# Optimization experiments

Measured on AMD Instinct MI355X. Metric: run time of the kernel, lower is better.

## Reference

```python
import jax, jax.numpy as jnp
import numpy as np

N = 100000
E = 1600000
NFEAT, NHID, NCLASS = 500, 128, 40


def setup_inputs() -> dict:
    key = jax.random.key(0)
    ks = jax.random.split(key, 12)
    x = jax.random.normal(ks[0], (N, NFEAT), dtype=jnp.float32)
    row = jax.random.randint(ks[1], (E,), 0, N, dtype=jnp.int32)
    col = jax.random.randint(ks[2], (E,), 0, N, dtype=jnp.int32)
    # precomputed normalized adjacency values (D^-1/2 A D^-1/2 style)
    edge_weight = jax.random.uniform(ks[3], (E,), dtype=jnp.float32) / 16.0
    def lin(k, fi, fo):
        s = 1.0 / np.sqrt(fi)
        return jax.random.uniform(k, (fi, fo), dtype=jnp.float32, minval=-s, maxval=s)
    return {
        "x": x, "row": row, "col": col, "edge_weight": edge_weight,
        "W1": lin(ks[4], NFEAT, NHID), "b1": jnp.zeros((NHID,), jnp.float32),
        "W2": lin(ks[5], NHID, NHID), "b2": jnp.zeros((NHID,), jnp.float32),
        "W3": lin(ks[6], NHID, NHID), "b3": jnp.zeros((NHID,), jnp.float32),
        "W4": lin(ks[7], NHID, NCLASS), "b4": jnp.zeros((NCLASS,), jnp.float32),
    }


def gcn_layer(h, row, col, edge_weight, W, b):
    # support = h @ W ; out = spmm(adj, support) + b  (Kipf GraphConvolution)
    support = h @ W                                   # [N, Fout]
    msgs = edge_weight[:, None] * support[col]        # [E, Fout] gather on source nodes
    agg = jax.ops.segment_sum(msgs, row, num_segments=N)  # scatter-add to dest nodes
    return agg + b


def reference(x, row, col, edge_weight, W1, b1, W2, b2, W3, b3, W4, b4):
    # dropout is identity in eval mode (training=False)
    h = jax.nn.relu(gcn_layer(x, row, col, edge_weight, W1, b1))
    h = jax.nn.relu(gcn_layer(h, row, col, edge_weight, W2, b2))
    h = jax.nn.relu(gcn_layer(h, row, col, edge_weight, W3, b3))
    h = gcn_layer(h, row, col, edge_weight, W4, b4)
    return jax.nn.log_softmax(h, axis=1)
```

## Files before the change

kernel.cpp:

```cpp
#include <hip/hip_runtime.h>
#include <cstdint>
#include <cstddef>

#define NFEAT 500
#define NHID  128
#define NCLASS 40

typedef __attribute__((ext_vector_type(8))) short bf16x8;
typedef __attribute__((ext_vector_type(4))) float f32x4;

__device__ __forceinline__ unsigned short f2bf(float f) {
    union { float f; unsigned u; } v; v.f = f;
    unsigned u = v.u;
    unsigned r = u + 0x7FFF + ((u >> 16) & 1);
    return (unsigned short)(r >> 16);
}
__device__ __forceinline__ float bf2f(unsigned short h) {
    union { unsigned u; float f; } v; v.u = ((unsigned)h) << 16; return v.f;
}


__global__ void k_hist(const int* __restrict__ row, int E, int* __restrict__ counts) {
    int i = blockIdx.x * 256 + threadIdx.x;
    if (i < E) atomicAdd(&counts[row[i]], 1);
}

__global__ void k_block_sum(const int* __restrict__ counts, int n, int* __restrict__ partials) {
    __shared__ int tmp[256];
    int i = blockIdx.x * 256 + threadIdx.x;
    tmp[threadIdx.x] = (i < n) ? counts[i] : 0;
    __syncthreads();
    for (int o = 128; o > 0; o >>= 1) {
        if (threadIdx.x < o) tmp[threadIdx.x] += tmp[threadIdx.x + o];
        __syncthreads();
    }
    if (threadIdx.x == 0) partials[blockIdx.x] = tmp[0];
}

__global__ void k_scan_partials(int* __restrict__ partials, int nb) {
    __shared__ int tmp[512];
    int t = threadIdx.x;
    int v = (t < nb) ? partials[t] : 0;
    tmp[t] = v;
    __syncthreads();
    for (int o = 1; o < 512; o <<= 1) {
        int add = (t >= o) ? tmp[t - o] : 0;
        __syncthreads();
        tmp[t] += add;
        __syncthreads();
    }
    if (t < nb) partials[t] = tmp[t] - v;
}

__global__ void k_scan_counts(int* __restrict__ counts, const int* __restrict__ partials,
                              int* __restrict__ row_ptr, int n) {
    __shared__ int tmp[256];
    int t = threadIdx.x;
    int i = blockIdx.x * 256 + t;
    int v = (i < n) ? counts[i] : 0;
    tmp[t] = v;
    __syncthreads();
    for (int o = 1; o < 256; o <<= 1) {
        int add = (t >= o) ? tmp[t - o] : 0;
        __syncthreads();
        tmp[t] += add;
        __syncthreads();
    }
    int incl = tmp[t];
    int base = partials[blockIdx.x];
    if (i < n) {
        row_ptr[i] = base + incl - v;
        counts[i] = 0;
    }
    if (i == n - 1) row_ptr[n] = base + incl;
}

__global__ void k_scatter(const int* __restrict__ row, const int* __restrict__ col,
                          const float* __restrict__ w, int E,
                          const int* __restrict__ row_ptr, int* __restrict__ cursor,
                          uint2* __restrict__ csr_cw) {
    int i = blockIdx.x * 256 + threadIdx.x;
    if (i < E) {
        int r = row[i];
        int p = row_ptr[r] + atomicAdd(&cursor[r], 1);
        csr_cw[p] = make_uint2((unsigned)col[i], __float_as_uint(w[i]));
    }
}


__global__ void k_prep_w(const float* __restrict__ W, unsigned short* __restrict__ Wt,
                         int K, int Norig, int Nt, int Kpad) {
    int idx = blockIdx.x * 256 + threadIdx.x;
    if (idx >= Nt * Kpad) return;
    int n = idx / Kpad, k = idx % Kpad;
    unsigned short v = 0;
    if (k < K && n < Norig) v = f2bf(W[(size_t)k * Norig + n]);
    Wt[idx] = v;
}


template<bool AFP32, int BN, int CN, int CPITCH>
__global__ __launch_bounds__(256) void k_gemm_mfma(const void* __restrict__ Ain,
                                                   const unsigned short* __restrict__ Wt,
                                                   unsigned short* __restrict__ C,
                                                   int M, int K, int Kpad) {
    constexpr int P  = 40;
    constexpr int NW = (BN == 128) ? 2 : 1;
    constexpr int MW = 4 / NW;
    constexpr int TM = 128 / (MW * 16);
    constexpr int TN = BN / (NW * 16);
    __shared__ unsigned short As[2][128][P];

    const int t = threadIdx.x;
    const int lane = t & 63;
    const int w = t >> 6;
    const int wm = w / NW, wn = w % NW;
    const int mbase = blockIdx.x * 128;
    const int l15 = lane & 15, quad = lane >> 4;

    const float* Af = (const float*)Ain;
    const unsigned short* Ab = (const unsigned short*)Ain;

    f32x4 acc[TM][TN];
#pragma unroll
    for (int mi = 0; mi < TM; mi++)
#pragma unroll
        for (int ni = 0; ni < TN; ni++)
            acc[mi][ni] = (f32x4){0.f, 0.f, 0.f, 0.f};

    float4 ra_f[4];
    uint4  ra_b[2];

    auto loadA = [&](int k0) {
        if (AFP32) {
#pragma unroll
            for (int p = 0; p < 4; p++) {
                int idx = p * 256 + t;
                int m = idx >> 3, ch = idx & 7;
                int gm = mbase + m, gk = k0 + ch * 4;
                float4 v = make_float4(0.f, 0.f, 0.f, 0.f);
                if (gm < M && gk + 4 <= K) v = *(const float4*)(Af + (size_t)gm * K + gk);
                ra_f[p] = v;
            }
        } else {
#pragma unroll
            for (int p = 0; p < 2; p++) {
                int idx = p * 256 + t;
                int m = idx >> 2, ch = idx & 3;
                ra_b[p] = *(const uint4*)(Ab + (size_t)(mbase + m) * Kpad + k0 + ch * 8);
            }
        }
    };
    auto storeLDS = [&](int buf) {
        if (AFP32) {
#pragma unroll
            for (int p = 0; p < 4; p++) {
                int idx = p * 256 + t;
                int m = idx >> 3, ch = idx & 7;
                float4 v = ra_f[p];
                unsigned long long pk = (unsigned long long)f2bf(v.x)
                                      | ((unsigned long long)f2bf(v.y) << 16)
                                      | ((unsigned long long)f2bf(v.z) << 32)
                                      | ((unsigned long long)f2bf(v.w) << 48);
                *(unsigned long long*)&As[buf][m][ch * 4] = pk;
            }
        } else {
#pragma unroll
            for (int p = 0; p < 2; p++) {
                int idx = p * 256 + t;
                int m = idx >> 2, ch = idx & 3;
                *(uint4*)&As[buf][m][ch * 8] = ra_b[p];
            }
        }
    };

    const int nIter = Kpad >> 5;
    loadA(0);
    storeLDS(0);
    __syncthreads();

    for (int it = 0; it < nIter; it++) {
        const int cur = it & 1;
        const int k0 = it << 5;
        const bool more = (it + 1) < nIter;
        if (more) loadA(k0 + 32);

        bf16x8 bfr[TN];
#pragma unroll
        for (int ni = 0; ni < TN; ni++)
            bfr[ni] = *(const bf16x8*)(Wt + (size_t)(wn * (TN * 16) + ni * 16 + l15) * Kpad + k0 + quad * 8);

        bf16x8 afr[TM];
#pragma unroll
        for (int mi = 0; mi < TM; mi++)
            afr[mi] = *(const bf16x8*)&As[cur][wm * (TM * 16) + mi * 16 + l15][quad * 8];

#pragma unroll
        for (int mi = 0; mi < TM; mi++)
#pragma unroll
            for (int ni = 0; ni < TN; ni++)
                acc[mi][ni] = __builtin_amdgcn_mfma_f32_16x16x32_bf16(afr[mi], bfr[ni], acc[mi][ni], 0, 0, 0);

        if (more) {
            storeLDS(cur ^ 1);
            __syncthreads();
        }
    }

#pragma unroll
    for (int mi = 0; mi < TM; mi++) {
#pragma unroll
        for (int r = 0; r < 4; r++) {
            int gm = mbase + wm * (TM * 16) + mi * 16 + quad * 4 + r;
#pragma unroll
            for (int ni = 0; ni < TN; ni++) {
                int gn = wn * (TN * 16) + ni * 16 + l15;
                if (gn < CN) C[(size_t)gm * CPITCH + gn] = f2bf(acc[mi][ni][r]);
            }
        }
    }
}


__global__ __launch_bounds__(256) void k_spmm128(const unsigned short* __restrict__ S,
                                                 const int* __restrict__ rp,
                                                 const uint2* __restrict__ cw,
                                                 const float* __restrict__ bias,
                                                 unsigned short* __restrict__ out,
                                                 int n, int do_relu) {
    int wid  = threadIdx.x >> 6;
    int lane = threadIdx.x & 63;
    int node = blockIdx.x * 4 + wid;
    if (node >= n) return;
    int s = rp[node], e = rp[node + 1];
    float a0x = 0.f, a0y = 0.f, a1x = 0.f, a1y = 0.f;
    float a2x = 0.f, a2y = 0.f, a3x = 0.f, a3y = 0.f;
    int i = s;
    for (; i + 4 <= e; i += 4) {
        uint2 e0 = cw[i], e1 = cw[i + 1], e2 = cw[i + 2], e3 = cw[i + 3];
        unsigned v0 = ((const unsigned*)(S + (size_t)e0.x * NHID))[lane];
        unsigned v1 = ((const unsigned*)(S + (size_t)e1.x * NHID))[lane];
        unsigned v2 = ((const unsigned*)(S + (size_t)e2.x * NHID))[lane];
        unsigned v3 = ((const unsigned*)(S + (size_t)e3.x * NHID))[lane];
        float w0 = __uint_as_float(e0.y), w1 = __uint_as_float(e1.y);
        float w2 = __uint_as_float(e2.y), w3 = __uint_as_float(e3.y);
        a0x = fmaf(w0, bf2f((unsigned short)v0), a0x); a0y = fmaf(w0, bf2f((unsigned short)(v0 >> 16)), a0y);
        a1x = fmaf(w1, bf2f((unsigned short)v1), a1x); a1y = fmaf(w1, bf2f((unsigned short)(v1 >> 16)), a1y);
        a2x = fmaf(w2, bf2f((unsigned short)v2), a2x); a2y = fmaf(w2, bf2f((unsigned short)(v2 >> 16)), a2y);
        a3x = fmaf(w3, bf2f((unsigned short)v3), a3x); a3y = fmaf(w3, bf2f((unsigned short)(v3 >> 16)), a3y);
    }
    for (; i < e; i++) {
        uint2 e0 = cw[i];
        unsigned v0 = ((const unsigned*)(S + (size_t)e0.x * NHID))[lane];
        float w0 = __uint_as_float(e0.y);
        a0x = fmaf(w0, bf2f((unsigned short)v0), a0x); a0y = fmaf(w0, bf2f((unsigned short)(v0 >> 16)), a0y);
    }
    float ax = (a0x + a1x) + (a2x + a3x) + bias[lane * 2];
    float ay = (a0y + a1y) + (a2y + a3y) + bias[lane * 2 + 1];
    if (do_relu) {
        ax = fmaxf(ax, 0.f);
        ay = fmaxf(ay, 0.f);
    }
    unsigned o = (unsigned)f2bf(ax) | ((unsigned)f2bf(ay) << 16);
    __builtin_nontemporal_store(o, (unsigned*)(out + (size_t)node * NHID) + lane);
}


__global__ __launch_bounds__(256) void k_spmm40_lsm(const unsigned short* __restrict__ S,
                                                    const int* __restrict__ rp,
                                                    const uint2* __restrict__ cw,
                                                    const float* __restrict__ bias,
                                                    float* __restrict__ out,
                                                    int n) {
    int wid  = threadIdx.x >> 6;
    int lane = threadIdx.x & 63;
    int node = blockIdx.x * 4 + wid;
    if (node >= n) return;
    int s = rp[node], e = rp[node + 1];
    float a0 = 0.f, a1 = 0.f, a2 = 0.f, a3 = 0.f;
    int i = s;
    bool act = lane < NCLASS;
    for (; i + 4 <= e; i += 4) {
        uint2 e0 = cw[i], e1 = cw[i + 1], e2 = cw[i + 2], e3 = cw[i + 3];
        if (act) {
            float v0 = bf2f(S[(size_t)e0.x * NCLASS + lane]);
            float v1 = bf2f(S[(size_t)e1.x * NCLASS + lane]);
            float v2 = bf2f(S[(size_t)e2.x * NCLASS + lane]);
            float v3 = bf2f(S[(size_t)e3.x * NCLASS + lane]);
            a0 = fmaf(__uint_as_float(e0.y), v0, a0);
            a1 = fmaf(__uint_as_float(e1.y), v1, a1);
            a2 = fmaf(__uint_as_float(e2.y), v2, a2);
            a3 = fmaf(__uint_as_float(e3.y), v3, a3);
        }
    }
    for (; i < e; i++) {
        uint2 e0 = cw[i];
        if (act) a0 = fmaf(__uint_as_float(e0.y), bf2f(S[(size_t)e0.x * NCLASS + lane]), a0);
    }
    float acc = (a0 + a1) + (a2 + a3);
    float logit = act ? acc + bias[lane] : -INFINITY;
    float m = logit;
#pragma unroll
    for (int o = 32; o >= 1; o >>= 1) m = fmaxf(m, __shfl_xor(m, o, 64));
    float ex = act ? expf(logit - m) : 0.f;
    float ssum = ex;
#pragma unroll
    for (int o = 32; o >= 1; o >>= 1) ssum += __shfl_xor(ssum, o, 64);
    if (act) {
        float r = logit - m - logf(ssum);
        __builtin_nontemporal_store(r, out + (size_t)node * NCLASS + lane);
    }
}


extern "C" void kernel_launch(void* const* d_in, const int* in_sizes, int n_in,
                              void* d_out, int out_size, void* d_ws, size_t ws_size,
                              hipStream_t stream) {
    const float* x  = (const float*)d_in[0];
    const int* row  = (const int*)d_in[1];
    const int* col  = (const int*)d_in[2];
    const float* ew = (const float*)d_in[3];
    const float* W1 = (const float*)d_in[4];
    const float* b1 = (const float*)d_in[5];
    const float* W2 = (const float*)d_in[6];
    const float* b2 = (const float*)d_in[7];
    const float* W3 = (const float*)d_in[8];
    const float* b3 = (const float*)d_in[9];
    const float* W4 = (const float*)d_in[10];
    const float* b4 = (const float*)d_in[11];
    float* out = (float*)d_out;

    const int Nn = in_sizes[0] / NFEAT;
    const int E  = in_sizes[1];
    const int NB = (Nn + 255) / 256;
    const int Mpad = (Nn + 127) & ~127;

    char* ws = (char*)d_ws;
    size_t off = 0;
    auto alloc = [&](size_t bytes) {
        size_t o = off;
        off = (off + bytes + 255) & ~(size_t)255;
        return o;
    };
    int*   row_ptr  = (int*)(ws + alloc((size_t)(Nn + 1) * 4));
    int*   counts   = (int*)(ws + alloc((size_t)Nn * 4));
    int*   partials = (int*)(ws + alloc((size_t)NB * 4));
    uint2* csr_cw   = (uint2*)(ws + alloc((size_t)E * 8));
    unsigned short* Sb  = (unsigned short*)(ws + alloc((size_t)Mpad * NHID * 2));
    unsigned short* Hb  = (unsigned short*)(ws + alloc((size_t)Mpad * NHID * 2));
    unsigned short* S4b = (unsigned short*)(ws + alloc((size_t)Mpad * NCLASS * 2));
    unsigned short* Wt1 = (unsigned short*)(ws + alloc((size_t)128 * 512 * 2));
    unsigned short* Wt2 = (unsigned short*)(ws + alloc((size_t)128 * 128 * 2));
    unsigned short* Wt3 = (unsigned short*)(ws + alloc((size_t)128 * 128 * 2));
    unsigned short* Wt4 = (unsigned short*)(ws + alloc((size_t)48 * 128 * 2));

    k_prep_w<<<(128 * 512 + 255) / 256, 256, 0, stream>>>(W1, Wt1, NFEAT, NHID, 128, 512);
    k_prep_w<<<(128 * 128 + 255) / 256, 256, 0, stream>>>(W2, Wt2, NHID, NHID, 128, 128);
    k_prep_w<<<(128 * 128 + 255) / 256, 256, 0, stream>>>(W3, Wt3, NHID, NHID, 128, 128);
    k_prep_w<<<(48 * 128 + 255) / 256, 256, 0, stream>>>(W4, Wt4, NHID, NCLASS, 48, 128);

    (void)hipMemsetAsync(counts, 0, (size_t)Nn * 4, stream);
    k_hist<<<(E + 255) / 256, 256, 0, stream>>>(row, E, counts);
    k_block_sum<<<NB, 256, 0, stream>>>(counts, Nn, partials);
    k_scan_partials<<<1, 512, 0, stream>>>(partials, NB);
    k_scan_counts<<<NB, 256, 0, stream>>>(counts, partials, row_ptr, Nn);
    k_scatter<<<(E + 255) / 256, 256, 0, stream>>>(row, col, ew, E, row_ptr, counts, csr_cw);

    const int gblocks = Mpad / 128;
    const int spmm_blocks = (Nn + 3) / 4;

    k_gemm_mfma<true, 128, 128, 128><<<gblocks, 256, 0, stream>>>(x, Wt1, Sb, Nn, NFEAT, 512);
    k_spmm128<<<spmm_blocks, 256, 0, stream>>>(Sb, row_ptr, csr_cw, b1, Hb, Nn, 1);
    k_gemm_mfma<false, 128, 128, 128><<<gblocks, 256, 0, stream>>>(Hb, Wt2, Sb, Nn, NHID, NHID);
    k_spmm128<<<spmm_blocks, 256, 0, stream>>>(Sb, row_ptr, csr_cw, b2, Hb, Nn, 1);
    k_gemm_mfma<false, 128, 128, 128><<<gblocks, 256, 0, stream>>>(Hb, Wt3, Sb, Nn, NHID, NHID);
    k_spmm128<<<spmm_blocks, 256, 0, stream>>>(Sb, row_ptr, csr_cw, b3, Hb, Nn, 1);
    k_gemm_mfma<false, 48, 40, 40><<<gblocks, 256, 0, stream>>>(Hb, Wt4, S4b, Nn, NHID, NHID);
    k_spmm40_lsm<<<spmm_blocks, 256, 0, stream>>>(S4b, row_ptr, csr_cw, b4, out, Nn);
}
```

Baseline: 860.1 us.

## Replace LDS-staged GEMM with direct register-fragment loads and double buffering

The GEMM no longer stages A tiles through shared memory with barriers. Each wave now loads its own MFMA A and B fragments straight from global memory into registers, with a two-set register double buffer, and computes a 32xBN slice covering the full N width. K is made a template constant so the loop can be fully unrolled. This removes LDS traffic and __syncthreads but makes each wave read all of W itself, and it relies on the cache for the strided per-lane row loads.

Result: slower. 893.2 us (+3.8%).

```diff
diff --git a/kernel.cpp b/kernel.cpp
--- a/kernel.cpp
+++ b/kernel.cpp
@@ -99,24 +99,19 @@
 }
 
 
-template<bool AFP32, int BN, int CN, int CPITCH>
-__global__ __launch_bounds__(256) void k_gemm_mfma(const void* __restrict__ Ain,
-                                                   const unsigned short* __restrict__ Wt,
-                                                   unsigned short* __restrict__ C,
-                                                   int M, int K, int Kpad) {
-    constexpr int P  = 40;
-    constexpr int NW = (BN == 128) ? 2 : 1;
-    constexpr int MW = 4 / NW;
-    constexpr int TM = 128 / (MW * 16);
-    constexpr int TN = BN / (NW * 16);
-    __shared__ unsigned short As[2][128][P];
-
+template<bool AFP32, int KPAD, int BN, int CN, int CPITCH>
+__global__ __launch_bounds__(256) void k_gemm_direct(const void* __restrict__ Ain,
+                                                     const unsigned short* __restrict__ Wt,
+                                                     unsigned short* __restrict__ C,
+                                                     int M, int K) {
+    constexpr int TM = 2;
+    constexpr int TN = BN / 16;
+    constexpr int NIT = KPAD / 32;
     const int t = threadIdx.x;
     const int lane = t & 63;
     const int w = t >> 6;
-    const int wm = w / NW, wn = w % NW;
-    const int mbase = blockIdx.x * 128;
     const int l15 = lane & 15, quad = lane >> 4;
+    const int rbase = blockIdx.x * 128 + w * 32;
 
     const float* Af = (const float*)Ain;
     const unsigned short* Ab = (const unsigned short*)Ain;
@@ -128,93 +123,77 @@
         for (int ni = 0; ni < TN; ni++)
             acc[mi][ni] = (f32x4){0.f, 0.f, 0.f, 0.f};
 
-    float4 ra_f[4];
-    uint4  ra_b[2];
-
-    auto loadA = [&](int k0) {
+    int rowi[TM];
+#pragma unroll
+    for (int mi = 0; mi < TM; mi++) {
+        int r = rbase + mi * 16 + l15;
+        rowi[mi] = AFP32 ? min(r, M - 1) : r;
+    }
+
+    float4 fA[2][TM][2];
+    bf16x8 hA[2][TM];
+    bf16x8 hB[2][TN];
+
+    auto loadA = [&](int set, int k0) {
         if (AFP32) {
-#pragma unroll
-            for (int p = 0; p < 4; p++) {
-                int idx = p * 256 + t;
-                int m = idx >> 3, ch = idx & 7;
-                int gm = mbase + m, gk = k0 + ch * 4;
-                float4 v = make_float4(0.f, 0.f, 0.f, 0.f);
-                if (gm < M && gk + 4 <= K) v = *(const float4*)(Af + (size_t)gm * K + gk);
-                ra_f[p] = v;
+            int gk = k0 + quad * 8;
+#pragma unroll
+            for (int mi = 0; mi < TM; mi++) {
+                const float* p = Af + (size_t)rowi[mi] * K + gk;
+                fA[set][mi][0] = (gk + 4 <= K) ? *(const float4*)p : make_float4(0.f, 0.f, 0.f, 0.f);
+                fA[set][mi][1] = (gk + 8 <= K) ? *(const float4*)(p + 4) : make_float4(0.f, 0.f, 0.f, 0.f);
             }
         } else {
 #pragma unroll
-            for (int p = 0; p < 2; p++) {
-                int idx = p * 256 + t;
-                int m = idx >> 2, ch = idx & 3;
-                ra_b[p] = *(const uint4*)(Ab + (size_t)(mbase + m) * Kpad + k0 + ch * 8);
+            for (int mi = 0; mi < TM; mi++)
+                hA[set][mi] = *(const bf16x8*)(Ab + (size_t)rowi[mi] * KPAD + k0 + quad * 8);
+        }
+    };
+    auto loadB = [&](int set, int k0) {
+#pragma unroll
+        for (int ni = 0; ni < TN; ni++)
+            hB[set][ni] = *(const bf16x8*)(Wt + (size_t)(ni * 16 + l15) * KPAD + k0 + quad * 8);
+    };
+    auto compute = [&](int set) {
+        bf16x8 afr[TM];
+#pragma unroll
+        for (int mi = 0; mi < TM; mi++) {
+            if (AFP32) {
+                float4 u = fA[set][mi][0], v = fA[set][mi][1];
+                bf16x8 r;
+                r[0] = (short)f2bf(u.x); r[1] = (short)f2bf(u.y);
+                r[2] = (short)f2bf(u.z); r[3] = (short)f2bf(u.w);
+                r[4] = (short)f2bf(v.x); r[5] = (short)f2bf(v.y);
+                r[6] = (short)f2bf(v.z); r[7] = (short)f2bf(v.w);
+                afr[mi] = r;
+            } else {
+                afr[mi] = hA[set][mi];
             }
         }
+#pragma unroll
+        for (int mi = 0; mi < TM; mi++)
+#pragma unroll
+            for (int ni = 0; ni < TN; ni++)
+                acc[mi][ni] = __builtin_amdgcn_mfma_f32_16x16x32_bf16(afr[mi], hB[set][ni], acc[mi][ni], 0, 0, 0);
     };
-    auto storeLDS = [&](int buf) {
-        if (AFP32) {
-#pragma unroll
-            for (int p = 0; p < 4; p++) {
-                int idx = p * 256 + t;
-                int m = idx >> 3, ch = idx & 7;
-                float4 v = ra_f[p];
-                unsigned long long pk = (unsigned long long)f2bf(v.x)
-                                      | ((unsigned long long)f2bf(v.y) << 16)
-                                      | ((unsigned long long)f2bf(v.z) << 32)
-                                      | ((unsigned long long)f2bf(v.w) << 48);
-                *(unsigned long long*)&As[buf][m][ch * 4] = pk;
-            }
-        } else {
-#pragma unroll
-            for (int p = 0; p < 2; p++) {
-                int idx = p * 256 + t;
-                int m = idx >> 2, ch = idx & 3;
-                *(uint4*)&As[buf][m][ch * 8] = ra_b[p];
-            }
-        }
-    };
-
-    const int nIter = Kpad >> 5;
-    loadA(0);
-    storeLDS(0);
-    __syncthreads();
-
-    for (int it = 0; it < nIter; it++) {
-        const int cur = it & 1;
-        const int k0 = it << 5;
-        const bool more = (it + 1) < nIter;
-        if (more) loadA(k0 + 32);
-
-        bf16x8 bfr[TN];
-#pragma unroll
-        for (int ni = 0; ni < TN; ni++)
-            bfr[ni] = *(const bf16x8*)(Wt + (size_t)(wn * (TN * 16) + ni * 16 + l15) * Kpad + k0 + quad * 8);
-
-        bf16x8 afr[TM];
-#pragma unroll
-        for (int mi = 0; mi < TM; mi++)
-            afr[mi] = *(const bf16x8*)&As[cur][wm * (TM * 16) + mi * 16 + l15][quad * 8];
-
-#pragma unroll
-        for (int mi = 0; mi < TM; mi++)
-#pragma unroll
-            for (int ni = 0; ni < TN; ni++)
-                acc[mi][ni] = __builtin_amdgcn_mfma_f32_16x16x32_bf16(afr[mi], bfr[ni], acc[mi][ni], 0, 0, 0);
-
-        if (more) {
-            storeLDS(cur ^ 1);
-            __syncthreads();
-        }
+
+    loadA(0, 0);
+    loadB(0, 0);
+    for (int it = 0; it < NIT; it += 2) {
+        if (it + 1 < NIT) { loadA(1, (it + 1) * 32); loadB(1, (it + 1) * 32); }
+        compute(0);
+        if (it + 2 < NIT) { loadA(0, (it + 2) * 32); loadB(0, (it + 2) * 32); }
+        if (it + 1 < NIT) compute(1);
     }
 
 #pragma unroll
     for (int mi = 0; mi < TM; mi++) {
 #pragma unroll
         for (int r = 0; r < 4; r++) {
-            int gm = mbase + wm * (TM * 16) + mi * 16 + quad * 4 + r;
+            int gm = rbase + mi * 16 + quad * 4 + r;
 #pragma unroll
             for (int ni = 0; ni < TN; ni++) {
-                int gn = wn * (TN * 16) + ni * 16 + l15;
+                int gn = ni * 16 + l15;
                 if (gn < CN) C[(size_t)gm * CPITCH + gn] = f2bf(acc[mi][ni][r]);
             }
         }
@@ -369,12 +348,12 @@
     const int gblocks = Mpad / 128;
     const int spmm_blocks = (Nn + 3) / 4;
 
-    k_gemm_mfma<true, 128, 128, 128><<<gblocks, 256, 0, stream>>>(x, Wt1, Sb, Nn, NFEAT, 512);
+    k_gemm_direct<true, 512, 128, 128, 128><<<gblocks, 256, 0, stream>>>(x, Wt1, Sb, Nn, NFEAT);
     k_spmm128<<<spmm_blocks, 256, 0, stream>>>(Sb, row_ptr, csr_cw, b1, Hb, Nn, 1);
-    k_gemm_mfma<false, 128, 128, 128><<<gblocks, 256, 0, stream>>>(Hb, Wt2, Sb, Nn, NHID, NHID);
+    k_gemm_direct<false, 128, 128, 128, 128><<<gblocks, 256, 0, stream>>>(Hb, Wt2, Sb, Nn, NHID);
     k_spmm128<<<spmm_blocks, 256, 0, stream>>>(Sb, row_ptr, csr_cw, b2, Hb, Nn, 1);
-    k_gemm_mfma<false, 128, 128, 128><<<gblocks, 256, 0, stream>>>(Hb, Wt3, Sb, Nn, NHID, NHID);
+    k_gemm_direct<false, 128, 128, 128, 128><<<gblocks, 256, 0, stream>>>(Hb, Wt3, Sb, Nn, NHID);
     k_spmm128<<<spmm_blocks, 256, 0, stream>>>(Sb, row_ptr, csr_cw, b3, Hb, Nn, 1);
-    k_gemm_mfma<false, 48, 40, 40><<<gblocks, 256, 0, stream>>>(Hb, Wt4, S4b, Nn, NHID, NHID);
+    k_gemm_direct<false, 128, 48, 40, 40><<<gblocks, 256, 0, stream>>>(Hb, Wt4, S4b, Nn, NHID);
     k_spmm40_lsm<<<spmm_blocks, 256, 0, stream>>>(S4b, row_ptr, csr_cw, b4, out, Nn);
 }
```
